# Performance work log

Measured on AMD Instinct MI355X. Metric: run time of the kernel, lower is better.

## Reference

```python
import jax, jax.numpy as jnp
import numpy as np

K = 3
EPS = 1e-5

def diff_conv(x, Tf, Tb, W, b):
    terms = [x]
    xf = x
    for _ in range(K):
        xf = jnp.einsum('mn,bnc->bmc', Tf, xf)
        terms.append(xf)
    xb = x
    for _ in range(K):
        xb = jnp.einsum('mn,bnc->bmc', Tb, xb)
        terms.append(xb)
    z = jnp.concatenate(terms, axis=-1)  # (B,N,(2K+1)*C)
    return z @ W + b

def layer_norm(x, gamma, beta):
    mu = jnp.mean(x, axis=-1, keepdims=True)
    var = jnp.var(x, axis=-1, keepdims=True)
    return (x - mu) * jax.lax.rsqrt(var + EPS) * gamma + beta

def dcgru_cell(x, h, Tf, Tb, Wg, bg, Wc, bc, gamma, beta):
    xh = jnp.concatenate([x, h], axis=-1)
    gates = jax.nn.sigmoid(diff_conv(xh, Tf, Tb, Wg, bg))
    r, u = jnp.split(gates, 2, axis=-1)
    xrh = jnp.concatenate([x, r * h], axis=-1)
    c = jnp.tanh(diff_conv(xrh, Tf, Tb, Wc, bc))
    h_new = (1.0 - u) * h + u * c
    return layer_norm(h_new, gamma, beta)

def setup_inputs() -> dict:
    key = jax.random.key(0)
    B, T, N, F, H = 32, 8, 512, 16, 128
    ks = jax.random.split(key, 16)
    s = 0.02
    n_terms = 2 * K + 1
    d0 = (F + H) * n_terms   # layer 0 combined diffusion dim
    d1 = (H + H) * n_terms   # layer 1
    inp = {
        'x_seq': jax.random.normal(ks[0], (B, T, N, F), dtype=jnp.float32),
        'T_f': jax.random.uniform(ks[1], (N, N), dtype=jnp.float32) / N,
        'T_b': jax.random.uniform(ks[2], (N, N), dtype=jnp.float32) / N,
        'Wg0': jax.random.normal(ks[3], (d0, 2 * H), dtype=jnp.float32) * s,
        'bg0': jnp.zeros((2 * H,), dtype=jnp.float32),
        'Wc0': jax.random.normal(ks[4], (d0, H), dtype=jnp.float32) * s,
        'bc0': jnp.zeros((H,), dtype=jnp.float32),
        'g0': jnp.ones((H,), dtype=jnp.float32),
        'be0': jnp.zeros((H,), dtype=jnp.float32),
        'Wg1': jax.random.normal(ks[5], (d1, 2 * H), dtype=jnp.float32) * s,
        'bg1': jnp.zeros((2 * H,), dtype=jnp.float32),
        'Wc1': jax.random.normal(ks[6], (d1, H), dtype=jnp.float32) * s,
        'bc1': jnp.zeros((H,), dtype=jnp.float32),
        'g1': jnp.ones((H,), dtype=jnp.float32),
        'be1': jnp.zeros((H,), dtype=jnp.float32),
    }
    return inp

def reference(x_seq, T_f, T_b, Wg0, bg0, Wc0, bc0, g0, be0, Wg1, bg1, Wc1, bc1, g1, be1):
    B, T, N, F = x_seq.shape
    H = g0.shape[0]
    h0 = jnp.zeros((B, N, H), dtype=x_seq.dtype)
    h1 = jnp.zeros((B, N, H), dtype=x_seq.dtype)

    def step(carry, x_t):
        h0, h1 = carry
        h0 = dcgru_cell(x_t, h0, T_f, T_b, Wg0, bg0, Wc0, bc0, g0, be0)
        h1 = dcgru_cell(h0, h1, T_f, T_b, Wg1, bg1, Wc1, bc1, g1, be1)
        return (h0, h1), None

    xs = jnp.swapaxes(x_seq, 0, 1)  # (T,B,N,F)
    (h0, h1), _ = jax.lax.scan(step, (h0, h1), xs)
    return (h0, h1)
```

## Files before the change

### kernel.cpp

```cpp
#include <hip/hip_runtime.h>
#include <hip/hip_bf16.h>
#include <math.h>

typedef unsigned short u16;
typedef __attribute__((ext_vector_type(8))) short short8;
typedef __attribute__((ext_vector_type(4))) float f32x4;

__device__ __forceinline__ u16 f2bf(float f) {
  union { float f; unsigned u; } v; v.f = f;
  unsigned r = v.u + 0x7fffu + ((v.u >> 16) & 1u);
  return (u16)(r >> 16);
}

__device__ __forceinline__ void glds16(const u16* g, u16* l) {
  __builtin_amdgcn_global_load_lds(
      (const __attribute__((address_space(1))) void*)g,
      (__attribute__((address_space(3))) void*)l, 16, 0, 0);
}

template<int N> __device__ __forceinline__ void kbar() {
  asm volatile("s_waitcnt vmcnt(%0)" :: "n"(N) : "memory");
  __builtin_amdgcn_s_barrier();
  asm volatile("" ::: "memory");
}
__device__ __forceinline__ void bar2() {
  asm volatile("" ::: "memory");
  __builtin_amdgcn_s_barrier();
  asm volatile("" ::: "memory");
}

template<int BM, int BN, int WR, int WC>
__device__ __forceinline__ void diff_body(
    u16* sm, int bx, int by, int bz,
    const u16* __restrict__ Tpow, const u16* __restrict__ zT,
    u16* __restrict__ zout, int ldz, int C, int coff0,
    u16* __restrict__ zdual, int Fdual)
{
  constexpr int BK = 64;
  constexpr int FM = BM / (WR * 16), FN = BN / (WC * 16);
  constexpr int SLOTS = (BM + 2 * BN) * 8;
  constexpr int NS = (SLOTS + 255) / 256;
  constexpr int VMIN = SLOTS / 256;
  constexpr int HALF = (BM + 2 * BN) * BK;
  const int tid = threadIdx.x, lane = tid & 63, wid = tid >> 6;
  const int wr = wid / WC, wc = wid % WC;
  const int l15 = lane & 15, l4 = lane >> 4;
  const int m0 = bx * BM;
  const int y0 = by * BN;
  const int b0 = (bz / 6) * 2, tc = bz % 6;
  const u16* A = Tpow + (long)tc * 262144;
  const int lb = (tid - lane) * 8;

  const u16* gp[NS];
  #pragma unroll
  for (int i = 0; i < NS; i++) {
    int s = tid + i * 256;
    if (s < BM * 8) {
      int row = s >> 3, kc = s & 7;
      gp[i] = A + (long)(m0 + row) * 512 + (kc ^ (row & 7)) * 8;
    } else {
      int s2 = s - BM * 8;
      int q = s2 / (BN * 8), n = (s2 % (BN * 8)) >> 3, kc = s2 & 7;
      gp[i] = zT + (long)(y0 + n) * 16384 + (b0 + q) * 512 + (kc ^ (n & 7)) * 8;
    }
  }

  auto stage = [&](int buf) {
    u16* base = sm + buf * HALF + lb;
    #pragma unroll
    for (int i = 0; i < NS; i++) {
      if (i * 256 + 256 <= SLOTS || tid < SLOTS - i * 256)
        glds16(gp[i], base + i * 2048);
    }
    #pragma unroll
    for (int i = 0; i < NS; i++) gp[i] += BK;
  };

  f32x4 acc[2][FM][FN] = {};
  auto compute = [&](int buf) {
    const u16* smc = sm + buf * HALF;
    #pragma unroll
    for (int kk = 0; kk < 2; kk++) {
      short8 af[FM], bf[2][FN];
      #pragma unroll
      for (int i = 0; i < FM; i++) {
        int ar = wr * FM * 16 + i * 16 + l15;
        af[i] = *(const short8*)&smc[ar * BK + (((kk * 4 + l4) ^ (ar & 7)) << 3)];
      }
      #pragma unroll
      for (int q = 0; q < 2; q++)
        #pragma unroll
        for (int j = 0; j < FN; j++) {
          int br = wc * FN * 16 + j * 16 + l15;
          bf[q][j] = *(const short8*)&smc[BM * BK + q * BN * BK + br * BK +
                                          (((kk * 4 + l4) ^ (br & 7)) << 3)];
        }
      #pragma unroll
      for (int q = 0; q < 2; q++)
        #pragma unroll
        for (int i = 0; i < FM; i++)
          #pragma unroll
          for (int j = 0; j < FN; j++)
            acc[q][i][j] = __builtin_amdgcn_mfma_f32_16x16x32_bf16(af[i], bf[q][j], acc[q][i][j], 0, 0, 0);
    }
  };

  stage(0);
  int cur = 0;
  for (int t = 0; t < 7; t++) {
    stage(cur ^ 1);
    kbar<VMIN>();
    compute(cur);
    bar2();
    cur ^= 1;
  }
  kbar<0>();
  compute(cur);

  const int tC = (1 + tc) * C;
  #pragma unroll
  for (int q = 0; q < 2; q++) {
    #pragma unroll
    for (int i = 0; i < FM; i++) {
      #pragma unroll
      for (int j = 0; j < FN; j++) {
        int node = m0 + wr * FM * 16 + i * 16 + l4 * 4;
        int ch = y0 + wc * FN * 16 + j * 16 + l15;
        #pragma unroll
        for (int rr = 0; rr < 4; rr++) {
          u16 v = f2bf(acc[q][i][j][rr]);
          long r = (long)(b0 + q) * 512 + node + rr;
          zout[r * ldz + tC + coff0 + ch] = v;
          if (Fdual && ch < Fdual) zdual[r * ldz + tC + ch] = v;
        }
      }
    }
  }
}

template<int BM, int BN, int WR, int WC>
__global__ __launch_bounds__(256, 2) void gemm_diff(
    const u16* __restrict__ Tpow, const u16* __restrict__ zT,
    u16* __restrict__ zout, int ldz, int C, int coff0,
    u16* __restrict__ zdual, int Fdual)
{
  __shared__ u16 sm[2 * (BM + 2 * BN) * 64];
  diff_body<BM, BN, WR, WC>(sm, blockIdx.x, blockIdx.y, blockIdx.z,
                            Tpow, zT, zout, ldz, C, coff0, zdual, Fdual);
}

__global__ __launch_bounds__(256, 2) void gdiff2(
    const u16* __restrict__ Tpow,
    const u16* __restrict__ zT1, u16* __restrict__ z1out, int y1sh, int r1cnt,
    const u16* __restrict__ zT0, u16* __restrict__ z0out, u16* __restrict__ z0dual)
{
  __shared__ u16 sm[2 * (128 + 2 * 64) * 64];
  int b = blockIdx.x;
  if (b < r1cnt) {
    int bx = b & 3, rem = b >> 2;
    int by = rem & ((1 << y1sh) - 1), bz = rem >> y1sh;
    diff_body<128, 64, 2, 2>(sm, bx, by, bz, Tpow, zT1, z1out, 1792, 256, 0, nullptr, 0);
  } else {
    int b2 = b - r1cnt;
    int bx = b2 & 3, rem = b2 >> 2;
    int by = rem % 3, bz = rem / 3;
    diff_body<128, 48, 4, 1>(sm, bx, by, bz, Tpow, zT0, z0out, 1024, 144, 0, z0dual, 16);
  }
}

__global__ __launch_bounds__(256, 2) void cdiff2(
    const u16* __restrict__ Tpow,
    const u16* __restrict__ zTc1, u16* __restrict__ z1c, int r1cnt,
    const u16* __restrict__ zTc0, u16* __restrict__ z0c)
{
  __shared__ u16 sm[2 * (128 + 2 * 64) * 64];
  int b = blockIdx.x;
  if (b < r1cnt) {
    int bx = b & 3, rem = b >> 2;
    int by = rem & 1, bz = rem >> 1;
    diff_body<128, 64, 2, 2>(sm, bx, by, bz, Tpow, zTc1, z1c, 1792, 256, 128, nullptr, 0);
  } else {
    int b2 = b - r1cnt;
    int bx = b2 & 3, rem = b2 >> 2;
    int by = rem & 1, bz = rem >> 1;
    diff_body<128, 64, 2, 2>(sm, bx, by, bz, Tpow, zTc0, z0c, 1024, 144, 16, nullptr, 0);
  }
}

template<int BM, int BN>
__device__ __forceinline__ void proj_body(
    u16* sm, int mb, int nb,
    const u16* __restrict__ Az, int ldA,
    const u16* __restrict__ W, int K,
    const float* __restrict__ bias, const float* __restrict__ hst,
    u16* __restrict__ zc, int ldzc, int Foff,
    u16* __restrict__ zTc, float* __restrict__ outbuf)
{
  constexpr int BK = 64;
  constexpr int FM = BM / 32, FN = BN / 32;
  constexpr int NSA = BM / 32, NSB = BN / 32;
  constexpr int VMIN = NSA + NSB;
  constexpr int HALF = (BM + BN) * BK;
  const int tid = threadIdx.x, lane = tid & 63, wid = tid >> 6;
  const int wr = wid >> 1, wc = wid & 1;
  const int l15 = lane & 15, l4 = lane >> 4;
  const int m0 = mb * BM;
  const int n0 = nb * BN;
  const int lb = (tid - lane) * 8;

  const u16* ap[NSA];
  const u16* wp[NSB];
  #pragma unroll
  for (int i = 0; i < NSA; i++) {
    int s = tid + i * 256;
    int row = s >> 3, kc = s & 7;
    ap[i] = Az + (long)(m0 + row) * ldA + (kc ^ (row & 7)) * 8;
  }
  #pragma unroll
  for (int i = 0; i < NSB; i++) {
    int s = tid + (NSA + i) * 256;
    int row = s >> 3, kc = s & 7;
    wp[i] = W + (long)(n0 + row - BM) * K + (kc ^ (row & 7)) * 8;
  }

  auto stage = [&](int buf) {
    u16* base = sm + buf * HALF + lb;
    #pragma unroll
    for (int i = 0; i < NSA; i++) { glds16(ap[i], base + i * 2048); ap[i] += BK; }
    #pragma unroll
    for (int i = 0; i < NSB; i++) { glds16(wp[i], base + (NSA + i) * 2048); wp[i] += BK; }
  };

  f32x4 acc[FM][FN] = {};
  auto compute = [&](int buf) {
    const u16* smc = sm + buf * HALF;
    #pragma unroll
    for (int kk = 0; kk < 2; kk++) {
      short8 af[FM], bf[FN];
      #pragma unroll
      for (int i = 0; i < FM; i++) {
        int ar = wr * FM * 16 + i * 16 + l15;
        af[i] = *(const short8*)&smc[ar * BK + (((kk * 4 + l4) ^ (ar & 7)) << 3)];
      }
      #pragma unroll
      for (int j = 0; j < FN; j++) {
        int br = wc * FN * 16 + j * 16 + l15;
        bf[j] = *(const short8*)&smc[BM * BK + br * BK + (((kk * 4 + l4) ^ (br & 7)) << 3)];
      }
      #pragma unroll
      for (int i = 0; i < FM; i++)
        #pragma unroll
        for (int j = 0; j < FN; j++)
          acc[i][j] = __builtin_amdgcn_mfma_f32_16x16x32_bf16(af[i], bf[j], acc[i][j], 0, 0, 0);
    }
  };

  stage(0);
  int cur = 0;
  const int NT = K >> 6;
  for (int t = 1; t < NT; t++) {
    stage(cur ^ 1);
    kbar<VMIN>();
    compute(cur);
    bar2();
    cur ^= 1;
  }
  kbar<0>();
  compute(cur);

  #pragma unroll
  for (int i = 0; i < FM; i++) {
    #pragma unroll
    for (int j = 0; j < FN; j++) {
      int mbv = m0 + wr * FM * 16 + i * 16 + l4 * 4;
      int n = n0 + wc * FN * 16 + j * 16 + l15;
      #pragma unroll
      for (int rr = 0; rr < 4; rr++) {
        float v = acc[i][j][rr] + bias[n];
        long r = mbv + rr;
        float g = 1.f / (1.f + expf(-v));
        if (n < 128) {
          float rh = g * hst[r * 128 + n];
          u16 hv = f2bf(rh);
          zc[r * ldzc + Foff + n] = hv;
          zTc[(long)n * 16384 + r] = hv;
        } else {
          outbuf[r * 128 + (n - 128)] = g;
        }
      }
    }
  }
}

__global__ __launch_bounds__(256) void gproj2(
    const u16* __restrict__ A1, int ldA1, const u16* __restrict__ W1, int K1,
    const float* __restrict__ b1, const float* __restrict__ h1s,
    u16* __restrict__ zc1, int Foff1, u16* __restrict__ zT1c, float* __restrict__ ub1,
    const u16* __restrict__ A0, const u16* __restrict__ W0,
    const float* __restrict__ b0, const float* __restrict__ h0s,
    u16* __restrict__ zc0, u16* __restrict__ zT0c, float* __restrict__ ub0)
{
  __shared__ u16 sm[2 * (64 + 64) * 64];
  int b = blockIdx.x;
  if (b < 1024) {
    proj_body<64, 64>(sm, b & 255, b >> 8, A1, ldA1, W1, K1, b1, h1s, zc1, ldA1, Foff1, zT1c, ub1);
  } else {
    int b2 = b - 1024;
    proj_body<64, 64>(sm, b2 & 255, b2 >> 8, A0, 1024, W0, 1024, b0, h0s, zc0, 1024, 16, zT0c, ub0);
  }
}

__global__ __launch_bounds__(256) void proj_cand_gru(
    const u16* __restrict__ Ag, const u16* __restrict__ Ac, int ldA,
    const u16* __restrict__ W, int K,
    const float* __restrict__ bias,
    const float* __restrict__ ub, float* __restrict__ h,
    const float* __restrict__ gamma, const float* __restrict__ beta,
    u16* __restrict__ rm0, int ld0, int co0,
    u16* __restrict__ rm1, int ld1, int co1,
    u16* __restrict__ cm0, int ro0,
    u16* __restrict__ cm1, int ro1,
    const float* __restrict__ xs, int tnext,
    u16* __restrict__ xz0g, u16* __restrict__ xz0c, u16* __restrict__ xz0T)
{
  constexpr int BM = 32, BN = 128, BK = 64;
  constexpr int FM = 2, FN = 2;
  constexpr int NSA = 1, NSB = 4;
  constexpr int HALF = (BM + BN) * BK;
  __shared__ u16 sm[2 * HALF];
  const int tid = threadIdx.x, lane = tid & 63, wid = tid >> 6;
  const int wc = wid;
  const int l15 = lane & 15, l4 = lane >> 4;
  const int m0 = blockIdx.x * BM;
  const int lb = (tid - lane) * 8;

  unsigned aoff[NSA];
  const u16* wp[NSB];
  #pragma unroll
  for (int i = 0; i < NSA; i++) {
    int s = tid + i * 256;
    int row = s >> 3, kc = s & 7;
    aoff[i] = (unsigned)((m0 + row) * ldA + (kc ^ (row & 7)) * 8);
  }
  #pragma unroll
  for (int i = 0; i < NSB; i++) {
    int s = tid + (NSA + i) * 256;
    int row = (s >> 3) - BM, kc = s & 7;
    wp[i] = W + (long)row * K + (kc ^ ((row + BM) & 7)) * 8;
  }

  auto stage = [&](int buf, int koff) {
    u16* base = sm + buf * HALF + lb;
    const u16* ab = ((koff >> 7) & 1) ? Ac : Ag;
    #pragma unroll
    for (int i = 0; i < NSA; i++) glds16(ab + aoff[i] + koff, base + i * 2048);
    #pragma unroll
    for (int i = 0; i < NSB; i++) { glds16(wp[i], base + (NSA + i) * 2048); wp[i] += BK; }
  };

  f32x4 acc[FM][FN] = {};
  auto compute = [&](int buf) {
    const u16* smc = sm + buf * HALF;
    #pragma unroll
    for (int kk = 0; kk < 2; kk++) {
      short8 af[FM], bf[FN];
      #pragma unroll
      for (int i = 0; i < FM; i++) {
        int ar = i * 16 + l15;
        af[i] = *(const short8*)&smc[ar * BK + (((kk * 4 + l4) ^ (ar & 7)) << 3)];
      }
      #pragma unroll
      for (int j = 0; j < FN; j++) {
        int br = wc * 32 + j * 16 + l15;
        bf[j] = *(const short8*)&smc[BM * BK + br * BK + (((kk * 4 + l4) ^ (br & 7)) << 3)];
      }
      #pragma unroll
      for (int i = 0; i < FM; i++)
        #pragma unroll
        for (int j = 0; j < FN; j++)
          acc[i][j] = __builtin_amdgcn_mfma_f32_16x16x32_bf16(af[i], bf[j], acc[i][j], 0, 0, 0);
    }
  };

  stage(0, 0);
  int cur = 0;
  const int NT = K >> 6;
  for (int t = 1; t < NT; t++) {
    stage(cur ^ 1, t * 64);
    kbar<5>();
    compute(cur);
    bar2();
    cur ^= 1;
  }
  kbar<0>();
  compute(cur);
  __syncthreads();

  float* hs = (float*)sm;
  #pragma unroll
  for (int i = 0; i < FM; i++) {
    #pragma unroll
    for (int j = 0; j < FN; j++) {
      #pragma unroll
      for (int rr = 0; rr < 4; rr++) {
        int lrow = i * 16 + l4 * 4 + rr;
        int n = wc * 32 + j * 16 + l15;
        long r = m0 + lrow;
        float c = tanhf(acc[i][j][rr] + bias[n]);
        float u = ub[r * 128 + n];
        float hold = h[r * 128 + n];
        hs[lrow * 132 + n] = (1.f - u) * hold + u * c;
      }
    }
  }
  __syncthreads();

  {
    int row = tid >> 3, g = tid & 7;
    float s = 0.f, s2 = 0.f;
    #pragma unroll
    for (int k = 0; k < 16; k++) {
      float v = hs[row * 132 + g + 8 * k];
      s += v; s2 += v * v;
    }
    s += __shfl_xor(s, 1); s2 += __shfl_xor(s2, 1);
    s += __shfl_xor(s, 2); s2 += __shfl_xor(s2, 2);
    s += __shfl_xor(s, 4); s2 += __shfl_xor(s2, 4);
    float mu = s * (1.f / 128.f);
    float var = s2 * (1.f / 128.f) - mu * mu;
    float rs = rsqrtf(var + 1e-5f);
    long rb = (long)(m0 + row) * 128;
    #pragma unroll
    for (int k = 0; k < 16; k++) {
      int c = g + 8 * k;
      float v = (hs[row * 132 + c] - mu) * rs * gamma[c] + beta[c];
      h[rb + c] = v;
      hs[row * 132 + c] = v;
    }
  }
  __syncthreads();

  #pragma unroll
  for (int i = 0; i < 16; i++) {
    int idx = tid + i * 256;
    int row = idx >> 7, c = idx & 127;
    u16 v = f2bf(hs[row * 132 + c]);
    long r = m0 + row;
    rm0[r * ld0 + co0 + c] = v;
    if (rm1) rm1[r * ld1 + co1 + c] = v;
  }
  {
    const int c2 = tid >> 1, half = tid & 1;
    u16 tmp[16];
    #pragma unroll
    for (int i = 0; i < 16; i++) tmp[i] = f2bf(hs[(half * 16 + i) * 132 + c2]);
    const short8* tv = (const short8*)tmp;
    long off = (long)(ro0 + c2) * 16384 + m0 + half * 16;
    *(short8*)&cm0[off] = tv[0];
    *(short8*)&cm0[off + 8] = tv[1];
    if (cm1) {
      long o2 = (long)(ro1 + c2) * 16384 + m0 + half * 16;
      *(short8*)&cm1[o2] = tv[0];
      *(short8*)&cm1[o2 + 8] = tv[1];
    }
  }
  if (xs) {
    for (int e = tid; e < 512; e += 256) {
      int lrow = e >> 4, f = e & 15;
      long r = m0 + lrow;
      int b = (int)(r >> 9), n = (int)(r & 511);
      u16 v = f2bf(xs[(((long)b * 8 + tnext) * 512 + n) * 16 + f]);
      xz0g[r * 1024 + f] = v;
      xz0c[r * 1024 + f] = v;
      xz0T[(long)f * 16384 + r] = v;
    }
  }
}

__global__ __launch_bounds__(256) void xk(
    const float* __restrict__ xs, int t,
    u16* __restrict__ z0g, u16* __restrict__ z0c, u16* __restrict__ z0Tg)
{
  int r = blockIdx.x * 256 + threadIdx.x;
  int b = r >> 9, n = r & 511;
  const float* src = xs + (((long)b * 8 + t) * 512 + n) * 16;
  u16 tmp[16];
  #pragma unroll
  for (int f = 0; f < 16; f++) tmp[f] = f2bf(src[f]);
  const short8* tv = (const short8*)tmp;
  *(short8*)&z0g[(long)r * 1024] = tv[0];
  *(short8*)&z0g[(long)r * 1024 + 8] = tv[1];
  *(short8*)&z0c[(long)r * 1024] = tv[0];
  *(short8*)&z0c[(long)r * 1024 + 8] = tv[1];
  #pragma unroll
  for (int f = 0; f < 16; f++) z0Tg[(long)f * 16384 + r] = tmp[f];
}

__global__ void cvtT(const float* __restrict__ Tf, const float* __restrict__ Tb,
                     u16* __restrict__ Tpow, u16* __restrict__ TfT, u16* __restrict__ TbT)
{
  int idx = blockIdx.x * 256 + threadIdx.x;
  int i = idx >> 9, j = idx & 511;
  const float* s = blockIdx.y ? Tb : Tf;
  u16* d = Tpow + (blockIdx.y ? 3 : 0) * 262144;
  u16* dT = blockIdx.y ? TbT : TfT;
  u16 v = f2bf(s[idx]);
  d[idx] = v;
  dT[(long)j * 512 + i] = v;
}

__global__ __launch_bounds__(256) void gemm_pow(
    const u16* __restrict__ A0, const u16* __restrict__ B0, u16* __restrict__ C0,
    const u16* __restrict__ A1, const u16* __restrict__ B1, u16* __restrict__ C1)
{
  constexpr int BM = 64, BN = 64, BK = 32;
  __shared__ u16 sm[(BM + BN) * BK];
  const int tid = threadIdx.x, lane = tid & 63, wid = tid >> 6;
  const int wr = wid >> 1, wc = wid & 1;
  const int l15 = lane & 15, l4 = lane >> 4;
  const int m0 = blockIdx.x * BM, n0 = blockIdx.y * BN;
  const u16* A = blockIdx.z ? A1 : A0;
  const u16* Bt = blockIdx.z ? B1 : B0;
  u16* Cc = blockIdx.z ? C1 : C0;

  f32x4 acc[2][2] = {};
  for (int k0 = 0; k0 < 512; k0 += BK) {
    for (int s = tid; s < (BM + BN) * 4; s += 256) {
      const u16* gp;
      if (s < BM * 4) { int m = s >> 2, kc = s & 3; gp = A + (long)(m0 + m) * 512 + k0 + kc * 8; }
      else { int q = s - BM * 4; int n = q >> 2, kc = q & 3; gp = Bt + (long)(n0 + n) * 512 + k0 + kc * 8; }
      glds16(gp, sm + (s - lane) * 8);
    }
    __syncthreads();
    short8 af[2], bf[2];
    #pragma unroll
    for (int i = 0; i < 2; i++)
      af[i] = *(const short8*)&sm[(wr * 32 + i * 16 + l15) * BK + l4 * 8];
    #pragma unroll
    for (int j = 0; j < 2; j++)
      bf[j] = *(const short8*)&sm[BM * BK + (wc * 32 + j * 16 + l15) * BK + l4 * 8];
    #pragma unroll
    for (int i = 0; i < 2; i++)
      #pragma unroll
      for (int j = 0; j < 2; j++)
        acc[i][j] = __builtin_amdgcn_mfma_f32_16x16x32_bf16(af[i], bf[j], acc[i][j], 0, 0, 0);
    __syncthreads();
  }
  #pragma unroll
  for (int i = 0; i < 2; i++)
    #pragma unroll
    for (int j = 0; j < 2; j++) {
      int mb = m0 + wr * 32 + i * 16 + l4 * 4;
      int n = n0 + wc * 32 + j * 16 + l15;
      #pragma unroll
      for (int rr = 0; rr < 4; rr++)
        Cc[(long)(mb + rr) * 512 + n] = f2bf(acc[i][j][rr]);
    }
}

__global__ void wt_cvt(const float* __restrict__ W, u16* __restrict__ Wt,
                       int Ksrc, int Kpad, int Nout) {
  long idx = (long)blockIdx.x * 256 + threadIdx.x;
  if (idx >= (long)Nout * Kpad) return;
  int o = (int)(idx / Kpad), k = (int)(idx % Kpad);
  Wt[idx] = f2bf(k < Ksrc ? W[(long)k * Nout + o] : 0.f);
}

extern "C" void kernel_launch(void* const* d_in, const int* in_sizes, int n_in,
                              void* d_out, int out_size, void* d_ws, size_t ws_size,
                              hipStream_t stream) {
  const float* x_seq = (const float*)d_in[0];
  const float* Tf  = (const float*)d_in[1];
  const float* Tb  = (const float*)d_in[2];
  const float* Wg0 = (const float*)d_in[3];
  const float* bg0 = (const float*)d_in[4];
  const float* Wc0 = (const float*)d_in[5];
  const float* bc0 = (const float*)d_in[6];
  const float* g0  = (const float*)d_in[7];
  const float* be0 = (const float*)d_in[8];
  const float* Wg1 = (const float*)d_in[9];
  const float* bg1 = (const float*)d_in[10];
  const float* Wc1 = (const float*)d_in[11];
  const float* bc1 = (const float*)d_in[12];
  const float* g1  = (const float*)d_in[13];
  const float* be1 = (const float*)d_in[14];

  constexpr long M = 16384;

  char* p = (char*)d_ws;
  auto carve = [&](size_t bytes) { char* r = p; p += (bytes + 255) & ~(size_t)255; return r; };
  u16* z0g  = (u16*)carve(M * 1024 * 2);
  u16* z0c  = (u16*)carve(M * 1024 * 2);
  u16* z1g  = (u16*)carve(M * 1792 * 2);
  u16* z1c  = (u16*)carve(M * 1792 * 2);
  u16* z0Tg = (u16*)carve(144L * M * 2);
  u16* z0Tc = (u16*)carve(128L * M * 2);
  u16* z1Tg = (u16*)carve(256L * M * 2);
  u16* z1Tc = (u16*)carve(128L * M * 2);
  float* ubuf0 = (float*)carve(M * 128 * 4);
  float* ubuf1 = (float*)carve(M * 128 * 4);
  u16* Tpow = (u16*)carve(6L * 512 * 512 * 2);
  u16* TfT  = (u16*)carve(512L * 512 * 2);
  u16* TbT  = (u16*)carve(512L * 512 * 2);
  u16* Wg0t = (u16*)carve(256L * 1024 * 2);
  u16* Wc0t = (u16*)carve(128L * 1024 * 2);
  u16* Wg1t = (u16*)carve(256L * 1792 * 2);
  u16* Wc1t = (u16*)carve(128L * 1792 * 2);

  float* h0 = (float*)d_out;
  float* h1 = h0 + M * 128;

  hipMemsetAsync(d_out, 0, (size_t)out_size * 4, stream);
  hipMemsetAsync(z0g, 0, (size_t)((char*)(z1c + M * 1792) - (char*)z0g), stream);
  hipMemsetAsync(z0Tg + 16L * M, 0, 128L * M * 2, stream);
  hipMemsetAsync(z1Tg + 128L * M, 0, 128L * M * 2, stream);

  cvtT<<<dim3(1024, 2), 256, 0, stream>>>(Tf, Tb, Tpow, TfT, TbT);
  gemm_pow<<<dim3(8, 8, 2), 256, 0, stream>>>(
      Tpow, TfT, Tpow + 1L * 262144, Tpow + 3L * 262144, TbT, Tpow + 4L * 262144);
  gemm_pow<<<dim3(8, 8, 2), 256, 0, stream>>>(
      Tpow + 1L * 262144, TfT, Tpow + 2L * 262144, Tpow + 4L * 262144, TbT, Tpow + 5L * 262144);
  wt_cvt<<<(256 * 1024 + 255) / 256, 256, 0, stream>>>(Wg0, Wg0t, 1008, 1024, 256);
  wt_cvt<<<(128 * 1024 + 255) / 256, 256, 0, stream>>>(Wc0, Wc0t, 1008, 1024, 128);
  wt_cvt<<<(256 * 1792 + 255) / 256, 256, 0, stream>>>(Wg1, Wg1t, 1792, 1792, 256);
  wt_cvt<<<(128 * 1792 + 255) / 256, 256, 0, stream>>>(Wc1, Wc1t, 1792, 1792, 128);

  xk<<<64, 256, 0, stream>>>(x_seq, 0, z0g, z0c, z0Tg);
  gemm_diff<128, 16, 4, 1><<<dim3(4, 1, 96), 256, 0, stream>>>(
      Tpow, z0Tg, z0g, 1024, 144, 0, z0c, 16);
  gproj2<<<1024, 256, 0, stream>>>(
      z0g, 1024, Wg0t, 1024, bg0, h0, z0c, 16, z0Tc, ubuf0,
      z0g, Wc0t, bc0, h0, z0c, z0Tc, ubuf0);
  proj_cand_gru<<<512, 256, 0, stream>>>(
      z0c, z0c, 1024, Wc0t, 1024, bc0, ubuf0, h0, g0, be0,
      z0g, 1024, 16, z1g, 1792, 0, z0Tg, 16, z1Tg, 0,
      x_seq, 1, z0g, z0c, z0Tg);

  for (int tt = 0; tt < 7; tt++) {
    int y1sh = (tt == 0) ? 1 : 2;
    int r1 = 4 * (1 << y1sh) * 96;
    gdiff2<<<r1 + 1152, 256, 0, stream>>>(
        Tpow, z1Tg, z1g, y1sh, r1, z0Tg, z0g, z0c);
    gproj2<<<2048, 256, 0, stream>>>(
        z1g, 1792, Wg1t, 1792, bg1, h1, z1c, 128, z1Tc, ubuf1,
        z0g, Wg0t, bg0, h0, z0c, z0Tc, ubuf0);
    int c1 = (tt == 0) ? 0 : 768;
    cdiff2<<<c1 + 768, 256, 0, stream>>>(
        Tpow, z1Tc, z1c, c1, z0Tc, z0c);
    proj_cand_gru<<<512, 256, 0, stream>>>(
        z1g, z1c, 1792, Wc1t, 1792, bc1, ubuf1, h1, g1, be1,
        z1g, 1792, 128, nullptr, 0, 0, z1Tg, 128, nullptr, 0,
        nullptr, 0, nullptr, nullptr, nullptr);
    proj_cand_gru<<<512, 256, 0, stream>>>(
        z0c, z0c, 1024, Wc0t, 1024, bc0, ubuf0, h0, g0, be0,
        z0g, 1024, 16, z1g, 1792, 0, z0Tg, 16, z1Tg, 0,
        (tt + 2 <= 7) ? x_seq : nullptr, tt + 2, z0g, z0c, z0Tg);
  }

  gdiff2<<<1536, 256, 0, stream>>>(Tpow, z1Tg, z1g, 2, 1536, z0Tg, z0g, z0c);
  gproj2<<<1024, 256, 0, stream>>>(
      z1g, 1792, Wg1t, 1792, bg1, h1, z1c, 128, z1Tc, ubuf1,
      z0g, Wg0t, bg0, h0, z0c, z0Tc, ubuf0);
  cdiff2<<<768, 256, 0, stream>>>(Tpow, z1Tc, z1c, 768, z0Tc, z0c);
  proj_cand_gru<<<512, 256, 0, stream>>>(
      z1g, z1c, 1792, Wc1t, 1792, bc1, ubuf1, h1, g1, be1,
      z1g, 1792, 128, nullptr, 0, 0, z1Tg, 128, nullptr, 0,
      nullptr, 0, nullptr, nullptr, nullptr);
}
```

Baseline: 1.397 ms.

## Fuse layer candidate kernels, double-buffer t0 slice, transpose zTc via LDS

The two per-step candidate/GRU projection launches for layers 1 and 0 are merged into one kernel (fused2) that splits its blocks between the two layers. The first 128/256 K-columns of the projection inputs now come from separate ping-pong t0 buffers, so the layers no longer write into each other's z arrays. The gate-projection epilogue also stages the r*h tile transpose through shared memory, so zTc is written with coalesced 16-byte stores instead of scattered 2-byte stores. This removes one launch per step and reduces strided global writes, at the cost of extra buffers, larger memsets and more complex indexing.

```diff
diff --git a/kernel.cpp b/kernel.cpp
--- a/kernel.cpp
+++ b/kernel.cpp
@@ -187,10 +187,11 @@
   }
 }
 
-template<int BM, int BN>
+template<int BM, int BN, bool SPLIT>
 __device__ __forceinline__ void proj_body(
     u16* sm, int mb, int nb,
     const u16* __restrict__ Az, int ldA,
+    const u16* __restrict__ t0, int t0ld,
     const u16* __restrict__ W, int K,
     const float* __restrict__ bias, const float* __restrict__ hst,
     u16* __restrict__ zc, int ldzc, int Foff,
@@ -208,13 +209,14 @@
   const int n0 = nb * BN;
   const int lb = (tid - lane) * 8;
 
-  const u16* ap[NSA];
+  long aoffA[NSA], aoffT[NSA];
   const u16* wp[NSB];
   #pragma unroll
   for (int i = 0; i < NSA; i++) {
     int s = tid + i * 256;
     int row = s >> 3, kc = s & 7;
-    ap[i] = Az + (long)(m0 + row) * ldA + (kc ^ (row & 7)) * 8;
+    aoffA[i] = (long)(m0 + row) * ldA + (kc ^ (row & 7)) * 8;
+    aoffT[i] = (long)(m0 + row) * t0ld + (kc ^ (row & 7)) * 8;
   }
   #pragma unroll
   for (int i = 0; i < NSB; i++) {
@@ -223,10 +225,14 @@
     wp[i] = W + (long)(n0 + row - BM) * K + (kc ^ (row & 7)) * 8;
   }
 
-  auto stage = [&](int buf) {
+  auto stage = [&](int buf, int koff) {
     u16* base = sm + buf * HALF + lb;
     #pragma unroll
-    for (int i = 0; i < NSA; i++) { glds16(ap[i], base + i * 2048); ap[i] += BK; }
+    for (int i = 0; i < NSA; i++) {
+      const u16* src = (SPLIT && koff < 256) ? t0 + aoffT[i] + koff
+                                             : Az + aoffA[i] + koff;
+      glds16(src, base + i * 2048);
+    }
     #pragma unroll
     for (int i = 0; i < NSB; i++) { glds16(wp[i], base + (NSA + i) * 2048); wp[i] += BK; }
   };
@@ -255,11 +261,11 @@
     }
   };
 
-  stage(0);
+  stage(0, 0);
   int cur = 0;
   const int NT = K >> 6;
   for (int t = 1; t < NT; t++) {
-    stage(cur ^ 1);
+    stage(cur ^ 1, t * 64);
     kbar<VMIN>();
     compute(cur);
     bar2();
@@ -268,6 +274,8 @@
   kbar<0>();
   compute(cur);
 
+  const bool rhpath = (n0 < 128);
+  u16 hv16[FM][FN][4];
   #pragma unroll
   for (int i = 0; i < FM; i++) {
     #pragma unroll
@@ -279,23 +287,47 @@
         float v = acc[i][j][rr] + bias[n];
         long r = mbv + rr;
         float g = 1.f / (1.f + expf(-v));
-        if (n < 128) {
+        if (rhpath) {
           float rh = g * hst[r * 128 + n];
           u16 hv = f2bf(rh);
           zc[r * ldzc + Foff + n] = hv;
-          zTc[(long)n * 16384 + r] = hv;
+          hv16[i][j][rr] = hv;
         } else {
           outbuf[r * 128 + (n - 128)] = g;
         }
       }
     }
   }
+  if (rhpath) {
+    bar2();
+    u16* tr = sm;
+    #pragma unroll
+    for (int i = 0; i < FM; i++)
+      #pragma unroll
+      for (int j = 0; j < FN; j++) {
+        int c = wc * FN * 16 + j * 16 + l15;
+        #pragma unroll
+        for (int rr = 0; rr < 4; rr++) {
+          int row = wr * FM * 16 + i * 16 + l4 * 4 + rr;
+          tr[c * 64 + (row ^ ((c & 7) << 3))] = hv16[i][j][rr];
+        }
+      }
+    __syncthreads();
+    int c = tid >> 2, rs = (tid & 3) << 4;
+    int swz = (c & 7) << 3;
+    long base = (long)(n0 + c) * 16384 + m0;
+    short8 v0 = *(const short8*)&tr[c * 64 + (rs ^ swz)];
+    short8 v1 = *(const short8*)&tr[c * 64 + ((rs + 8) ^ swz)];
+    *(short8*)&zTc[base + rs] = v0;
+    *(short8*)&zTc[base + rs + 8] = v1;
+  }
 }
 
 __global__ __launch_bounds__(256) void gproj2(
-    const u16* __restrict__ A1, int ldA1, const u16* __restrict__ W1, int K1,
+    const u16* __restrict__ A1, int ldA1, const u16* __restrict__ t01, int t0ld1,
+    const u16* __restrict__ W1, int K1,
     const float* __restrict__ b1, const float* __restrict__ h1s,
-    u16* __restrict__ zc1, int Foff1, u16* __restrict__ zT1c, float* __restrict__ ub1,
+    u16* __restrict__ zc1, int ldzc1, int Foff1, u16* __restrict__ zT1c, float* __restrict__ ub1,
     const u16* __restrict__ A0, const u16* __restrict__ W0,
     const float* __restrict__ b0, const float* __restrict__ h0s,
     u16* __restrict__ zc0, u16* __restrict__ zT0c, float* __restrict__ ub0)
@@ -303,15 +335,18 @@
   __shared__ u16 sm[2 * (64 + 64) * 64];
   int b = blockIdx.x;
   if (b < 1024) {
-    proj_body<64, 64>(sm, b & 255, b >> 8, A1, ldA1, W1, K1, b1, h1s, zc1, ldA1, Foff1, zT1c, ub1);
+    proj_body<64, 64, true>(sm, b & 255, b >> 8, A1, ldA1, t01, t0ld1, W1, K1,
+                            b1, h1s, zc1, ldzc1, Foff1, zT1c, ub1);
   } else {
     int b2 = b - 1024;
-    proj_body<64, 64>(sm, b2 & 255, b2 >> 8, A0, 1024, W0, 1024, b0, h0s, zc0, 1024, 16, zT0c, ub0);
-  }
-}
-
-__global__ __launch_bounds__(256) void proj_cand_gru(
+    proj_body<64, 64, false>(sm, b2 & 255, b2 >> 8, A0, 1024, nullptr, 0, W0, 1024,
+                             b0, h0s, zc0, 1024, 16, zT0c, ub0);
+  }
+}
+
+__device__ __forceinline__ void cand_body(int blk,
     const u16* __restrict__ Ag, const u16* __restrict__ Ac, int ldA,
+    const u16* __restrict__ t0, int t0ld,
     const u16* __restrict__ W, int K,
     const float* __restrict__ bias,
     const float* __restrict__ ub, float* __restrict__ h,
@@ -321,26 +356,27 @@
     u16* __restrict__ cm0, int ro0,
     u16* __restrict__ cm1, int ro1,
     const float* __restrict__ xs, int tnext,
-    u16* __restrict__ xz0g, u16* __restrict__ xz0c, u16* __restrict__ xz0T)
+    u16* __restrict__ xz0g, u16* __restrict__ xz0c, u16* __restrict__ xz0T,
+    u16* sm)
 {
   constexpr int BM = 32, BN = 128, BK = 64;
   constexpr int FM = 2, FN = 2;
   constexpr int NSA = 1, NSB = 4;
   constexpr int HALF = (BM + BN) * BK;
-  __shared__ u16 sm[2 * HALF];
   const int tid = threadIdx.x, lane = tid & 63, wid = tid >> 6;
   const int wc = wid;
   const int l15 = lane & 15, l4 = lane >> 4;
-  const int m0 = blockIdx.x * BM;
+  const int m0 = blk * BM;
   const int lb = (tid - lane) * 8;
 
-  unsigned aoff[NSA];
+  long aoffA[NSA], aoffT[NSA];
   const u16* wp[NSB];
   #pragma unroll
   for (int i = 0; i < NSA; i++) {
     int s = tid + i * 256;
     int row = s >> 3, kc = s & 7;
-    aoff[i] = (unsigned)((m0 + row) * ldA + (kc ^ (row & 7)) * 8);
+    aoffA[i] = (long)(m0 + row) * ldA + (kc ^ (row & 7)) * 8;
+    aoffT[i] = (long)(m0 + row) * t0ld + (kc ^ (row & 7)) * 8;
   }
   #pragma unroll
   for (int i = 0; i < NSB; i++) {
@@ -351,9 +387,13 @@
 
   auto stage = [&](int buf, int koff) {
     u16* base = sm + buf * HALF + lb;
-    const u16* ab = ((koff >> 7) & 1) ? Ac : Ag;
-    #pragma unroll
-    for (int i = 0; i < NSA; i++) glds16(ab + aoff[i] + koff, base + i * 2048);
+    #pragma unroll
+    for (int i = 0; i < NSA; i++) {
+      const u16* src;
+      if (koff < 128) src = t0 + aoffT[i] + koff;
+      else src = (((koff >> 7) & 1) ? Ac : Ag) + aoffA[i] + koff;
+      glds16(src, base + i * 2048);
+    }
     #pragma unroll
     for (int i = 0; i < NSB; i++) { glds16(wp[i], base + (NSA + i) * 2048); wp[i] += BK; }
   };
@@ -474,6 +514,44 @@
       xz0c[r * 1024 + f] = v;
       xz0T[(long)f * 16384 + r] = v;
     }
+  }
+}
+
+__global__ __launch_bounds__(256) void fused1(
+    const u16* Ag, const u16* Ac, int ldA, const u16* t0, int t0ld,
+    const u16* W, int K, const float* bias,
+    const float* ub, float* h, const float* gamma, const float* beta,
+    u16* rm0, int ld0, int co0, u16* rm1, int ld1, int co1,
+    u16* cm0, int ro0, u16* cm1, int ro1,
+    const float* xs, int tnext, u16* xz0g, u16* xz0c, u16* xz0T)
+{
+  __shared__ u16 sm[2 * (32 + 128) * 64];
+  cand_body(blockIdx.x, Ag, Ac, ldA, t0, t0ld, W, K, bias, ub, h, gamma, beta,
+            rm0, ld0, co0, rm1, ld1, co1, cm0, ro0, cm1, ro1,
+            xs, tnext, xz0g, xz0c, xz0T, sm);
+}
+
+__global__ __launch_bounds__(256) void fused2(
+    const u16* Ag1, const u16* Ac1, int ldA1, const u16* t01, int t0ld1,
+    const u16* W1, int K1, const float* bias1,
+    const float* ub1, float* h1p, const float* g1p, const float* be1p,
+    u16* rm01, int ld01, int co01, u16* cm01, int ro01,
+    const u16* A0, const u16* t00, const u16* W0, const float* bias0,
+    const float* ub0, float* h0p, const float* g0p, const float* be0p,
+    u16* rm00, int co00, u16* rm10, int ld10, int co10,
+    u16* cm00, int ro00, u16* cm10, int ro10,
+    const float* xs, int tnext, u16* xz0g, u16* xz0c, u16* xz0T)
+{
+  __shared__ u16 sm[2 * (32 + 128) * 64];
+  int b = blockIdx.x;
+  if (b < 512) {
+    cand_body(b, Ag1, Ac1, ldA1, t01, t0ld1, W1, K1, bias1, ub1, h1p, g1p, be1p,
+              rm01, ld01, co01, nullptr, 0, 0, cm01, ro01, nullptr, 0,
+              nullptr, 0, nullptr, nullptr, nullptr, sm);
+  } else {
+    cand_body(b - 512, A0, A0, 1024, t00, 1024, W0, 1024, bias0, ub0, h0p, g0p, be0p,
+              rm00, 1024, co00, rm10, ld10, co10, cm00, ro00, cm10, ro10,
+              xs, tnext, xz0g, xz0c, xz0T, sm);
   }
 }
 
@@ -593,6 +671,8 @@
   u16* z0c  = (u16*)carve(M * 1024 * 2);
   u16* z1g  = (u16*)carve(M * 1792 * 2);
   u16* z1c  = (u16*)carve(M * 1792 * 2);
+  u16* t0A  = (u16*)carve(M * 256 * 2);
+  u16* t0B  = (u16*)carve(M * 256 * 2);
   u16* z0Tg = (u16*)carve(144L * M * 2);
   u16* z0Tc = (u16*)carve(128L * M * 2);
   u16* z1Tg = (u16*)carve(256L * M * 2);
@@ -611,7 +691,7 @@
   float* h1 = h0 + M * 128;
 
   hipMemsetAsync(d_out, 0, (size_t)out_size * 4, stream);
-  hipMemsetAsync(z0g, 0, (size_t)((char*)(z1c + M * 1792) - (char*)z0g), stream);
+  hipMemsetAsync(z0g, 0, (size_t)((char*)(t0B + M * 256) - (char*)z0g), stream);
   hipMemsetAsync(z0Tg + 16L * M, 0, 128L * M * 2, stream);
   hipMemsetAsync(z1Tg + 128L * M, 0, 128L * M * 2, stream);
 
@@ -629,41 +709,45 @@
   gemm_diff<128, 16, 4, 1><<<dim3(4, 1, 96), 256, 0, stream>>>(
       Tpow, z0Tg, z0g, 1024, 144, 0, z0c, 16);
   gproj2<<<1024, 256, 0, stream>>>(
-      z0g, 1024, Wg0t, 1024, bg0, h0, z0c, 16, z0Tc, ubuf0,
-      z0g, Wc0t, bc0, h0, z0c, z0Tc, ubuf0);
-  proj_cand_gru<<<512, 256, 0, stream>>>(
-      z0c, z0c, 1024, Wc0t, 1024, bc0, ubuf0, h0, g0, be0,
-      z0g, 1024, 16, z1g, 1792, 0, z0Tg, 16, z1Tg, 0,
+      z0g, 1024, z0g, 1024, Wg0t, 1024, bg0, h0, z0c, 1024, 16, z0Tc, ubuf0,
+      z0g, Wg0t, bg0, h0, z0c, z0Tc, ubuf0);
+  fused1<<<512, 256, 0, stream>>>(
+      z0c, z0c, 1024, z0c, 1024, Wc0t, 1024, bc0, ubuf0, h0, g0, be0,
+      z0g, 1024, 16, t0A, 256, 0, z0Tg, 16, z1Tg, 0,
       x_seq, 1, z0g, z0c, z0Tg);
 
-  for (int tt = 0; tt < 7; tt++) {
-    int y1sh = (tt == 0) ? 1 : 2;
+  for (int s = 0; s < 7; s++) {
+    u16* t0c = (s & 1) ? t0B : t0A;
+    u16* t0n = (s & 1) ? t0A : t0B;
+    int y1sh = (s == 0) ? 1 : 2;
     int r1 = 4 * (1 << y1sh) * 96;
     gdiff2<<<r1 + 1152, 256, 0, stream>>>(
         Tpow, z1Tg, z1g, y1sh, r1, z0Tg, z0g, z0c);
     gproj2<<<2048, 256, 0, stream>>>(
-        z1g, 1792, Wg1t, 1792, bg1, h1, z1c, 128, z1Tc, ubuf1,
+        z1g, 1792, t0c, 256, Wg1t, 1792, bg1, h1, z1c, 1792, 128, z1Tc, ubuf1,
         z0g, Wg0t, bg0, h0, z0c, z0Tc, ubuf0);
-    int c1 = (tt == 0) ? 0 : 768;
+    int c1 = (s == 0) ? 0 : 768;
     cdiff2<<<c1 + 768, 256, 0, stream>>>(
         Tpow, z1Tc, z1c, c1, z0Tc, z0c);
-    proj_cand_gru<<<512, 256, 0, stream>>>(
-        z1g, z1c, 1792, Wc1t, 1792, bc1, ubuf1, h1, g1, be1,
-        z1g, 1792, 128, nullptr, 0, 0, z1Tg, 128, nullptr, 0,
+    fused2<<<1024, 256, 0, stream>>>(
+        z1g, z1c, 1792, t0c, 256, Wc1t, 1792, bc1, ubuf1, h1, g1, be1,
+        t0n, 256, 128, z1Tg, 128,
+        z0c, z0c, Wc0t, bc0, ubuf0, h0, g0, be0,
+        z0g, 16, t0n, 256, 0, z0Tg, 16, z1Tg, 0,
+        (s + 2 <= 7) ? x_seq : nullptr, s + 2, z0g, z0c, z0Tg);
+  }
+
+  {
+    u16* t0c = t0B;
+    u16* t0n = t0A;
+    gdiff2<<<1536, 256, 0, stream>>>(Tpow, z1Tg, z1g, 2, 1536, z0Tg, z0g, z0c);
+    gproj2<<<1024, 256, 0, stream>>>(
+        z1g, 1792, t0c, 256, Wg1t, 1792, bg1, h1, z1c, 1792, 128, z1Tc, ubuf1,
+        z0g, Wg0t, bg0, h0, z0c, z0Tc, ubuf0);
+    cdiff2<<<768, 256, 0, stream>>>(Tpow, z1Tc, z1c, 768, z0Tc, z0c);
+    fused1<<<512, 256, 0, stream>>>(
+        z1g, z1c, 1792, t0c, 256, Wc1t, 1792, bc1, ubuf1, h1, g1, be1,
+        t0n, 256, 128, nullptr, 0, 0, z1Tg, 128, nullptr, 0,
         nullptr, 0, nullptr, nullptr, nullptr);
-    proj_cand_gru<<<512, 256, 0, stream>>>(
-        z0c, z0c, 1024, Wc0t, 1024, bc0, ubuf0, h0, g0, be0,
-        z0g, 1024, 16, z1g, 1792, 0, z0Tg, 16, z1Tg, 0,
-        (tt + 2 <= 7) ? x_seq : nullptr, tt + 2, z0g, z0c, z0Tg);
-  }
-
-  gdiff2<<<1536, 256, 0, stream>>>(Tpow, z1Tg, z1g, 2, 1536, z0Tg, z0g, z0c);
-  gproj2<<<1024, 256, 0, stream>>>(
-      z1g, 1792, Wg1t, 1792, bg1, h1, z1c, 128, z1Tc, ubuf1,
-      z0g, Wg0t, bg0, h0, z0c, z0Tc, ubuf0);
-  cdiff2<<<768, 256, 0, stream>>>(Tpow, z1Tc, z1c, 768, z0Tc, z0c);
-  proj_cand_gru<<<512, 256, 0, stream>>>(
-      z1g, z1c, 1792, Wc1t, 1792, bc1, ubuf1, h1, g1, be1,
-      z1g, 1792, 128, nullptr, 0, 0, z1Tg, 128, nullptr, 0,
-      nullptr, 0, nullptr, nullptr, nullptr);
-}
+  }
+}
```

After: 1.360 ms. -2.7%, faster.
